# Optimization experiments

Measured on AMD Instinct MI355X. Metric: run time of the kernel, lower is better.

## Reference

```python
import jax, jax.numpy as jnp
import numpy as np

K = 512  # number of largest entries to KEEP per row (module's k)


def _topk_keep(x, k):
    """Zero all but the k largest entries along the last axis.

    Matches torch: topk(-x, dim-k) finds the (dim-k) smallest values of x
    and scatters 0 into them, keeping the k largest. We implement the
    equivalent keep-mask via top_k indices of x itself (ties resolved by
    index order, same as torch.topk).
    """
    shp = x.shape
    d = shp[-1]
    x2 = x.reshape(-1, d)                      # [N, d]
    _, idx = jax.lax.top_k(x2, k)              # [N, k] indices of largest
    rows = jnp.arange(x2.shape[0])[:, None]    # [N, 1]
    mask = jnp.zeros_like(x2).at[rows, idx].set(1.0)
    return (x2 * mask).reshape(shp)


def setup_inputs() -> dict:
    key = jax.random.key(0)
    x = jax.random.normal(key, (4, 4096, 4096), dtype=jnp.float32)
    return {"x": x}


def reference(x):
    return _topk_keep(x, K)
```

## Files before the change

### kernel.cpp

```cpp
#include <hip/hip_runtime.h>

#define D     4096
#define KKEEP 512
#define TPB   256
#define EPT   16

__device__ __forceinline__ unsigned key_of(float f) {
    unsigned u = __float_as_uint(f);
    return (u & 0x80000000u) ? ~u : (u | 0x80000000u);
}
__device__ __forceinline__ float val_of(unsigned k) {
    unsigned u = (k & 0x80000000u) ? (k ^ 0x80000000u) : ~k;
    return __uint_as_float(u);
}

__global__ __launch_bounds__(TPB, 8)
void topk_keep_kernel(const float* __restrict__ x, float* __restrict__ out) {
    const int tid = threadIdx.x;
    const long base = (long)blockIdx.x * D + (long)tid * EPT;

    unsigned k[EPT];
    {
        const float4* px = (const float4*)(x + base);
        float4 f0 = px[0], f1 = px[1], f2 = px[2], f3 = px[3];
        k[ 0]=key_of(f0.x); k[ 1]=key_of(f0.y); k[ 2]=key_of(f0.z); k[ 3]=key_of(f0.w);
        k[ 4]=key_of(f1.x); k[ 5]=key_of(f1.y); k[ 6]=key_of(f1.z); k[ 7]=key_of(f1.w);
        k[ 8]=key_of(f2.x); k[ 9]=key_of(f2.y); k[10]=key_of(f2.z); k[11]=key_of(f2.w);
        k[12]=key_of(f3.x); k[13]=key_of(f3.y); k[14]=key_of(f3.z); k[15]=key_of(f3.w);
    }

    __shared__ unsigned hist[256];
    __shared__ unsigned s_sel[2];
    __shared__ unsigned s_wsum[TPB / 64];

    unsigned prefix = 0;
    unsigned rem = KKEEP;

    #pragma unroll
    for (int r = 0; r < 4; ++r) {
        const int shift = 24 - 8 * r;
        hist[tid] = 0;
        __syncthreads();

        if (r == 0) {
            #pragma unroll
            for (int j = 0; j < EPT; ++j)
                atomicAdd(&hist[k[j] >> 24], 1u);
        } else {
            const int hs = shift + 8;
            #pragma unroll
            for (int j = 0; j < EPT; ++j)
                if ((k[j] >> hs) == (prefix >> hs))
                    atomicAdd(&hist[(k[j] >> shift) & 255u], 1u);
        }
        __syncthreads();

        if (tid < 64) {
            unsigned c0 = hist[tid * 4 + 0], c1 = hist[tid * 4 + 1];
            unsigned c2 = hist[tid * 4 + 2], c3 = hist[tid * 4 + 3];
            unsigned lt = c0 + c1 + c2 + c3;
            unsigned s = lt;
            #pragma unroll
            for (int off = 1; off < 64; off <<= 1) {
                unsigned t = __shfl_down(s, off, 64);
                if (tid + off < 64) s += t;
            }
            unsigned sx = s - lt;
            unsigned si3 = sx + c3;
            unsigned si2 = si3 + c2;
            unsigned si1 = si2 + c1;
            unsigned si0 = si1 + c0;
            if (si3 >= rem && si3 - c3 < rem) { s_sel[0] = tid * 4 + 3; s_sel[1] = rem - (si3 - c3); }
            if (si2 >= rem && si2 - c2 < rem) { s_sel[0] = tid * 4 + 2; s_sel[1] = rem - (si2 - c2); }
            if (si1 >= rem && si1 - c1 < rem) { s_sel[0] = tid * 4 + 1; s_sel[1] = rem - (si1 - c1); }
            if (si0 >= rem && si0 - c0 < rem) { s_sel[0] = tid * 4 + 0; s_sel[1] = rem - (si0 - c0); }
        }
        __syncthreads();
        prefix |= s_sel[0] << shift;
        rem = s_sel[1];
    }

    const unsigned tkey = prefix;

    unsigned cnt_eq = 0;
    #pragma unroll
    for (int j = 0; j < EPT; ++j) cnt_eq += (k[j] == tkey) ? 1u : 0u;

    const unsigned lane = tid & 63u, wid = (unsigned)tid >> 6;
    unsigned incl = cnt_eq;
    #pragma unroll
    for (int off = 1; off < 64; off <<= 1) {
        unsigned t = __shfl_up(incl, off, 64);
        if (lane >= (unsigned)off) incl += t;
    }
    if (lane == 63) s_wsum[wid] = incl;
    __syncthreads();
    unsigned ebase = incl - cnt_eq;
    #pragma unroll
    for (unsigned w = 0; w < TPB / 64; ++w)
        if (w < wid) ebase += s_wsum[w];

    float4 o[4];
    float* of = (float*)o;
    unsigned eqr = ebase;
    #pragma unroll
    for (int j = 0; j < EPT; ++j) {
        bool keep;
        if (k[j] > tkey)       keep = true;
        else if (k[j] == tkey) { keep = (eqr < rem); ++eqr; }
        else                   keep = false;
        of[j] = keep ? val_of(k[j]) : 0.0f;
    }
    float4* po = (float4*)(out + base);
    po[0] = o[0]; po[1] = o[1]; po[2] = o[2]; po[3] = o[3];
}

extern "C" void kernel_launch(void* const* d_in, const int* in_sizes, int n_in,
                              void* d_out, int out_size, void* d_ws, size_t ws_size,
                              hipStream_t stream) {
    const float* x = (const float*)d_in[0];
    float* out = (float*)d_out;
    const int rows = in_sizes[0] / D;
    topk_keep_kernel<<<dim3(rows), dim3(TPB), 0, stream>>>(x, out);
}
```

Before: 453.5 us.

## Use three radix-select passes with 2048-bin padded histograms instead of four

The per-row radix select now runs three passes over 11/11/10-bit digits instead of four 8-bit passes, with a 2048-bin shared histogram padded to avoid bank conflicts. The prefix scan to find the threshold bin is spread across all 256 threads, using per-wave totals in shared memory. This cuts one round of histogram clearing, atomics and barriers. In exchange each pass clears and scans a larger histogram and adds an extra barrier, and shared memory per block grows.

After: 436.1 us. 3.8% less time.

```diff
diff --git a/kernel.cpp b/kernel.cpp
--- a/kernel.cpp
+++ b/kernel.cpp
@@ -4,6 +4,10 @@
 #define KKEEP 512
 #define TPB   256
 #define EPT   16
+#define NB    2048
+#define BPT   (NB / TPB)
+#define HA(d) ((d) + ((d) >> 3))
+#define HWORDS (NB + NB / 8)
 
 __device__ __forceinline__ unsigned key_of(float f) {
     unsigned u = __float_as_uint(f);
@@ -18,6 +22,7 @@
 void topk_keep_kernel(const float* __restrict__ x, float* __restrict__ out) {
     const int tid = threadIdx.x;
     const long base = (long)blockIdx.x * D + (long)tid * EPT;
+    const unsigned lane = tid & 63u, wid = (unsigned)tid >> 6;
 
     unsigned k[EPT];
     {
@@ -29,51 +34,64 @@
         k[12]=key_of(f3.x); k[13]=key_of(f3.y); k[14]=key_of(f3.z); k[15]=key_of(f3.w);
     }
 
-    __shared__ unsigned hist[256];
+    __shared__ unsigned hist[HWORDS];
+    __shared__ unsigned s_wtot[4];
     __shared__ unsigned s_sel[2];
-    __shared__ unsigned s_wsum[TPB / 64];
+    __shared__ unsigned s_wsum[4];
 
     unsigned prefix = 0;
     unsigned rem = KKEEP;
 
     #pragma unroll
-    for (int r = 0; r < 4; ++r) {
-        const int shift = 24 - 8 * r;
-        hist[tid] = 0;
+    for (int r = 0; r < 3; ++r) {
+        const int shift = (r == 0) ? 21 : (r == 1) ? 10 : 0;
+        const unsigned mask = (r == 2) ? 1023u : 2047u;
+
+        #pragma unroll
+        for (int i = 0; i < 9; ++i) hist[tid + i * TPB] = 0;
         __syncthreads();
 
         if (r == 0) {
             #pragma unroll
             for (int j = 0; j < EPT; ++j)
-                atomicAdd(&hist[k[j] >> 24], 1u);
+                atomicAdd(&hist[HA(k[j] >> 21)], 1u);
         } else {
-            const int hs = shift + 8;
+            const int hs = (r == 1) ? 21 : 10;
             #pragma unroll
             for (int j = 0; j < EPT; ++j)
                 if ((k[j] >> hs) == (prefix >> hs))
-                    atomicAdd(&hist[(k[j] >> shift) & 255u], 1u);
+                    atomicAdd(&hist[HA((k[j] >> shift) & mask)], 1u);
         }
         __syncthreads();
 
-        if (tid < 64) {
-            unsigned c0 = hist[tid * 4 + 0], c1 = hist[tid * 4 + 1];
-            unsigned c2 = hist[tid * 4 + 2], c3 = hist[tid * 4 + 3];
-            unsigned lt = c0 + c1 + c2 + c3;
-            unsigned s = lt;
+        unsigned c[BPT];
+        unsigned ct = 0;
+        {
+            const int hb = tid * 9;
             #pragma unroll
-            for (int off = 1; off < 64; off <<= 1) {
-                unsigned t = __shfl_down(s, off, 64);
-                if (tid + off < 64) s += t;
+            for (int i = 0; i < BPT; ++i) { c[i] = hist[hb + i]; ct += c[i]; }
+        }
+        unsigned s = ct;
+        #pragma unroll
+        for (int off = 1; off < 64; off <<= 1) {
+            unsigned t = __shfl_down(s, off, 64);
+            if (lane + (unsigned)off < 64u) s += t;
+        }
+        if (lane == 0) s_wtot[wid] = s;
+        __syncthreads();
+        unsigned above = s - ct;
+        #pragma unroll
+        for (unsigned w = 0; w < 4; ++w)
+            if (w > wid) above += s_wtot[w];
+        unsigned run = above;
+        #pragma unroll
+        for (int i = BPT - 1; i >= 0; --i) {
+            unsigned incl = run + c[i];
+            if (incl >= rem && run < rem) {
+                s_sel[0] = (unsigned)(tid * BPT + i);
+                s_sel[1] = rem - run;
             }
-            unsigned sx = s - lt;
-            unsigned si3 = sx + c3;
-            unsigned si2 = si3 + c2;
-            unsigned si1 = si2 + c1;
-            unsigned si0 = si1 + c0;
-            if (si3 >= rem && si3 - c3 < rem) { s_sel[0] = tid * 4 + 3; s_sel[1] = rem - (si3 - c3); }
-            if (si2 >= rem && si2 - c2 < rem) { s_sel[0] = tid * 4 + 2; s_sel[1] = rem - (si2 - c2); }
-            if (si1 >= rem && si1 - c1 < rem) { s_sel[0] = tid * 4 + 1; s_sel[1] = rem - (si1 - c1); }
-            if (si0 >= rem && si0 - c0 < rem) { s_sel[0] = tid * 4 + 0; s_sel[1] = rem - (si0 - c0); }
+            run = incl;
         }
         __syncthreads();
         prefix |= s_sel[0] << shift;
@@ -86,7 +104,6 @@
     #pragma unroll
     for (int j = 0; j < EPT; ++j) cnt_eq += (k[j] == tkey) ? 1u : 0u;
 
-    const unsigned lane = tid & 63u, wid = (unsigned)tid >> 6;
     unsigned incl = cnt_eq;
     #pragma unroll
     for (int off = 1; off < 64; off <<= 1) {
@@ -97,7 +114,7 @@
     __syncthreads();
     unsigned ebase = incl - cnt_eq;
     #pragma unroll
-    for (unsigned w = 0; w < TPB / 64; ++w)
+    for (unsigned w = 0; w < 4; ++w)
         if (w < wid) ebase += s_wsum[w];
 
     float4 o[4];
```
